# Performance work log

Measured on AMD Instinct MI355X. Metric: run time of the kernel, lower is better.

The kernel has to match this reference:

```python
import jax, jax.numpy as jnp
import numpy as np

D_MODEL, D_STATE, EXPAND = 256, 16, 2
D_INNER = EXPAND * D_MODEL
DT_RANK = (D_MODEL + 15) // 16
BATCH, SEQLEN = 4, 4096


def silu(x):
    return x * jax.nn.sigmoid(x)


def setup_inputs() -> dict:
    key = jax.random.key(0)
    ks = jax.random.split(key, 10)
    h = jax.random.normal(ks[0], (BATCH, SEQLEN, D_MODEL), dtype=jnp.float32)
    Wi_f = jax.random.normal(ks[1], (2 * D_INNER, D_MODEL), dtype=jnp.float32) / np.sqrt(D_MODEL)
    Wi_b = jax.random.normal(ks[2], (2 * D_INNER, D_MODEL), dtype=jnp.float32) / np.sqrt(D_MODEL)
    Wx_f = jax.random.normal(ks[3], (DT_RANK + 2 * D_STATE, D_INNER), dtype=jnp.float32) / np.sqrt(D_INNER)
    Wx_b = jax.random.normal(ks[4], (DT_RANK + 2 * D_STATE, D_INNER), dtype=jnp.float32) / np.sqrt(D_INNER)
    dt_std = DT_RANK ** -0.5
    Wdt_f = jax.random.uniform(ks[5], (D_INNER, DT_RANK), dtype=jnp.float32, minval=-dt_std, maxval=dt_std)
    Wdt_b = jax.random.uniform(ks[6], (D_INNER, DT_RANK), dtype=jnp.float32, minval=-dt_std, maxval=dt_std)
    # dt bias = inverse-softplus of dt sampled log-uniform in [1e-3, 1e-1]
    dt = jnp.exp(jax.random.uniform(ks[7], (D_INNER,), dtype=jnp.float32) * (np.log(0.1) - np.log(0.001)) + np.log(0.001))
    dt = jnp.clip(dt, 1e-4, None)
    inv_dt = dt + jnp.log(-jnp.expm1(-dt))
    bdt_f = inv_dt
    bdt_b = inv_dt
    A_log = jnp.log(jnp.broadcast_to(jnp.arange(1, D_STATE + 1, dtype=jnp.float32), (D_INNER, D_STATE)))
    A_log_f = A_log
    A_log_b = A_log
    D_f = jnp.ones((D_INNER,), dtype=jnp.float32)
    D_b = jnp.ones((D_INNER,), dtype=jnp.float32)
    Wo = jax.random.normal(ks[8], (D_MODEL, 2 * D_INNER), dtype=jnp.float32) / np.sqrt(2 * D_INNER)
    return {"hidden_states": h, "Wi_f": Wi_f, "Wi_b": Wi_b, "Wx_f": Wx_f, "Wx_b": Wx_b,
            "Wdt_f": Wdt_f, "Wdt_b": Wdt_b, "bdt_f": bdt_f, "bdt_b": bdt_b,
            "A_log_f": A_log_f, "A_log_b": A_log_b, "D_f": D_f, "D_b": D_b, "Wo": Wo}


def mamba_dir(h, Wi, Wx, Wdt, bdt, A_log, Dp, reverse):
    b, l, _ = h.shape
    di, r = Wdt.shape
    n = A_log.shape[1]
    xz = h @ Wi.T                      # [b,l,2*di]
    if reverse:
        xz = xz[:, ::-1]
    x, z = xz[..., :di], xz[..., di:]
    u = silu(x)                        # selective_scan input u
    x_dbl = u @ Wx.T                   # [b,l,r+2n]
    delta = jax.nn.softplus(x_dbl[..., :r] @ Wdt.T + bdt)   # [b,l,di]
    Bm = x_dbl[..., r:r + n]           # [b,l,n]
    Cm = x_dbl[..., r + n:r + 2 * n]   # [b,l,n]
    A = -jnp.exp(A_log)                # [di,n]

    def step(s, inp):
        u_t, d_t, B_t, C_t = inp       # [b,di],[b,di],[b,n],[b,n]
        dA = jnp.exp(d_t[..., None] * A)                         # [b,di,n]
        s = dA * s + (d_t * u_t)[..., None] * B_t[:, None, :]    # [b,di,n]
        y_t = jnp.einsum('bdn,bn->bd', s, C_t)
        return s, y_t

    s0 = jnp.zeros((b, di, n), dtype=u.dtype)
    xs = (jnp.swapaxes(u, 0, 1), jnp.swapaxes(delta, 0, 1),
          jnp.swapaxes(Bm, 0, 1), jnp.swapaxes(Cm, 0, 1))
    _, ys = jax.lax.scan(step, s0, xs)
    y = jnp.swapaxes(ys, 0, 1) + u * Dp          # skip term D*u
    y = y * silu(z)                              # gated output
    if reverse:
        y = y[:, ::-1]
    return y


def reference(hidden_states, Wi_f, Wi_b, Wx_f, Wx_b, Wdt_f, Wdt_b, bdt_f, bdt_b, A_log_f, A_log_b, D_f, D_b, Wo):
    y_f = mamba_dir(hidden_states, Wi_f, Wx_f, Wdt_f, bdt_f, A_log_f, D_f, False)
    y_b = mamba_dir(hidden_states, Wi_b, Wx_b, Wdt_b, bdt_b, A_log_b, D_b, True)
    y = jnp.concatenate([y_f, y_b], axis=-1)     # [b,l,2*di]
    return y @ Wo.T                              # [b,l,d_model]
```

## Files before the change

### kernel.cpp

```cpp
#include <hip/hip_runtime.h>
#include <hip/hip_bf16.h>
#include <cstddef>
#include <cstdint>

#define D_MODELc 256
#define D_STATEc 16
#define D_INNERc 512
#define DT_RANKc 16
#define BATCHc   4
#define SEQLENc  4096
#define NCHUNK   128
#define CHUNK    32

typedef unsigned short u16;
typedef __attribute__((ext_vector_type(8))) short bf16x8;
typedef __attribute__((ext_vector_type(4))) float f32x4;
typedef float __attribute__((ext_vector_type(4))) f4v;

__device__ __forceinline__ float siluf(float v) { return v / (1.f + __expf(-v)); }

__device__ __forceinline__ u16 bf16_rne(float f) {
    uint32_t u = __float_as_uint(f);
    u += 0x7fffu + ((u >> 16) & 1u);
    return (u16)(u >> 16);
}
__device__ __forceinline__ float bf16_to_f(u16 h) {
    return __uint_as_float(((uint32_t)h) << 16);
}
__device__ __forceinline__ uint32_t pack_hl(float f) {
    u16 hh = bf16_rne(f);
    u16 ll = bf16_rne(f - bf16_to_f(hh));
    return ((uint32_t)hh << 16) | ll;
}
__device__ __forceinline__ float unpack_add(uint32_t v) {
    return __uint_as_float(v & 0xFFFF0000u) + __uint_as_float(v << 16);
}
__device__ __forceinline__ void unpack_frag(const uint32_t* q, bf16x8& fh, bf16x8& fl) {
    union { bf16x8 v; uint32_t w[4]; } H, L;
    #pragma unroll
    for (int i = 0; i < 4; i++) {
        uint32_t a = q[2 * i], b = q[2 * i + 1];
        H.w[i] = (a >> 16) | (b & 0xFFFF0000u);
        L.w[i] = (a & 0xFFFFu) | (b << 16);
    }
    fh = H.v; fl = L.v;
}
__device__ __forceinline__ float softplusf(float x) {
    return fmaxf(x, 0.f) + __logf(1.f + __expf(-fabsf(x)));
}

#define GLL16(g, l) __builtin_amdgcn_global_load_lds( \
    (const __attribute__((address_space(1))) uint32_t*)(g), \
    (__attribute__((address_space(3))) uint32_t*)(l), 16, 0, 0)

__global__ __launch_bounds__(256) void split_kernel(const float* __restrict__ in,
                                                    u16* __restrict__ hi,
                                                    u16* __restrict__ lo, int n4) {
    int i = blockIdx.x * 256 + threadIdx.x;
    const int stride = gridDim.x * 256;
    for (; i < n4; i += stride) {
        float4 v = ((const float4*)in)[i];
        u16 h0 = bf16_rne(v.x), h1 = bf16_rne(v.y), h2 = bf16_rne(v.z), h3 = bf16_rne(v.w);
        ushort4 hv; hv.x = h0; hv.y = h1; hv.z = h2; hv.w = h3;
        ushort4 lv;
        lv.x = bf16_rne(v.x - bf16_to_f(h0));
        lv.y = bf16_rne(v.y - bf16_to_f(h1));
        lv.z = bf16_rne(v.z - bf16_to_f(h2));
        lv.w = bf16_rne(v.w - bf16_to_f(h3));
        ((ushort4*)hi)[i] = hv;
        ((ushort4*)lo)[i] = lv;
    }
}

template<int EPI, int NBL2, int AINT>
__global__ __launch_bounds__(256) void gemm_mfma(
        const u16* __restrict__ Ah, const u16* __restrict__ Al, int lda,
        const u16* __restrict__ Bh, const u16* __restrict__ Bl, int ldb,
        float* __restrict__ out0,
        uint32_t* __restrict__ uhl,
        int M, int N, int K) {
    __shared__ char lds[2][32768];
    const int t    = threadIdx.x;
    const int lane = t & 63;
    const int wid  = t >> 6;
    const int wrow = wid >> 1, wcol = wid & 1;

    const int id  = blockIdx.x;
    const int xcd = id & 7;
    const int j   = id >> 3;
    const int nb  = j & ((1 << NBL2) - 1);
    const int mg  = j >> NBL2;
    const int m0  = (mg * 8 + xcd) * 128;
    const int n0  = nb * 128;

    const int lr  = lane & 15;
    const int kgl = lane >> 4;

    f32x4 acc[4][4] = {};

    auto stage = [&](int buf, int k0) {
        if (AINT == 0) {
            #pragma unroll
            for (int i = 0; i < 8; i++) {
                int c    = i * 256 + t;
                int tile = c >> 9;
                int kg   = (c >> 7) & 3;
                int row  = c & 127;
                const u16* bsrc = (tile == 0) ? Ah : (tile == 1) ? Al : (tile == 2) ? Bh : Bl;
                int r0 = (tile < 2) ? m0 : n0;
                int ld = (tile < 2) ? lda : ldb;
                const u16* g = bsrc + (size_t)(r0 + row) * ld + k0 + kg * 8;
                GLL16(g, &lds[buf][c * 16]);
            }
        } else {
            const uint32_t* Aint = (const uint32_t*)Ah;
            #pragma unroll
            for (int i = 0; i < 8; i++) {
                int c = i * 256 + t;
                if (c < 1024) {
                    int kg   = c >> 8;
                    int row  = (c >> 1) & 127;
                    int half = c & 1;
                    const uint32_t* g = Aint + (size_t)(m0 + row) * lda + k0 + kg * 8 + half * 4;
                    GLL16(g, &lds[buf][c * 16]);
                } else {
                    int cb   = c - 1024;
                    int tile = cb >> 9;
                    int kg   = (cb >> 7) & 3;
                    int row  = cb & 127;
                    const u16* bsrc = tile ? Bl : Bh;
                    const u16* g = bsrc + (size_t)(n0 + row) * ldb + k0 + kg * 8;
                    GLL16(g, &lds[buf][c * 16]);
                }
            }
        }
    };

    const int NT = K >> 5;
    stage(0, 0);
    __syncthreads();

    for (int kt = 0; kt < NT; ++kt) {
        const int buf = kt & 1;
        if (kt + 1 < NT) stage(buf ^ 1, (kt + 1) * 32);

        bf16x8 afh[4], afl[4];
        if (AINT == 0) {
            const u16* lb = (const u16*)lds[buf];
            #pragma unroll
            for (int mi = 0; mi < 4; mi++) {
                int row = wrow * 64 + mi * 16 + lr;
                afh[mi] = *(const bf16x8*)(lb + 0 * 4096 + kgl * 1024 + row * 8);
                afl[mi] = *(const bf16x8*)(lb + 1 * 4096 + kgl * 1024 + row * 8);
            }
        } else {
            const uint32_t* la = (const uint32_t*)lds[buf];
            #pragma unroll
            for (int mi = 0; mi < 4; mi++) {
                int row = wrow * 64 + mi * 16 + lr;
                unpack_frag(la + kgl * 1024 + row * 8, afh[mi], afl[mi]);
            }
        }
        const u16* lbB = (const u16*)(lds[buf] + 16384);
        #pragma unroll
        for (int ni = 0; ni < 4; ni++) {
            int row = wcol * 64 + ni * 16 + lr;
            bf16x8 bfh = *(const bf16x8*)(lbB + 0 * 4096 + kgl * 1024 + row * 8);
            bf16x8 bfl = *(const bf16x8*)(lbB + 1 * 4096 + kgl * 1024 + row * 8);
            #pragma unroll
            for (int mi = 0; mi < 4; mi++) {
                acc[mi][ni] = __builtin_amdgcn_mfma_f32_16x16x32_bf16(afh[mi], bfh, acc[mi][ni], 0, 0, 0);
                acc[mi][ni] = __builtin_amdgcn_mfma_f32_16x16x32_bf16(afh[mi], bfl, acc[mi][ni], 0, 0, 0);
                acc[mi][ni] = __builtin_amdgcn_mfma_f32_16x16x32_bf16(afl[mi], bfh, acc[mi][ni], 0, 0, 0);
            }
        }
        __syncthreads();
    }

    #pragma unroll
    for (int mi = 0; mi < 4; mi++) {
        #pragma unroll
        for (int ni = 0; ni < 4; ni++) {
            #pragma unroll
            for (int r = 0; r < 4; r++) {
                int m = m0 + wrow * 64 + mi * 16 + kgl * 4 + r;
                int n = n0 + wcol * 64 + ni * 16 + lr;
                float v = acc[mi][ni][r];
                if (EPI == 0) {
                    __builtin_nontemporal_store(v, &out0[(size_t)m * N + n]);
                } else {
                    float s = siluf(v);
                    int dirn = n >> 10;
                    int nn   = n & 1023;
                    size_t dof = (size_t)dirn * (size_t)M * 512;
                    if (nn < 512) {
                        uhl[dof + (size_t)m * 512 + nn] = pack_hl(s);
                    } else {
                        out0[dof + (size_t)m * 512 + (nn - 512)] = s;
                    }
                }
            }
        }
    }
}

__global__ __launch_bounds__(256) void xdbl_mfma(
        const uint32_t* __restrict__ Uhl,
        const u16* __restrict__ WxH, const u16* __restrict__ WxL,
        float* __restrict__ out) {
    __shared__ uint32_t lds[4][64][8];
    const int t    = threadIdx.x;
    const int lane = t & 63;
    const int wid  = t >> 6;
    const int m0   = blockIdx.x * 64;
    const int dir  = blockIdx.y;
    const int Mp   = gridDim.x * 64;
    const int lr   = lane & 15;
    const int kgl  = lane >> 4;

    const size_t dofU = (size_t)dir * (size_t)Mp * 512;
    const size_t dofW = (size_t)dir * (size_t)48 * 512;

    f32x4 acc[3] = {};

    for (int k0 = 0; k0 < 512; k0 += 32) {
        #pragma unroll
        for (int i = 0; i < 2; i++) {
            int c    = i * 256 + t;
            int kg   = c >> 7;
            int row  = (c >> 1) & 63;
            int half = c & 1;
            const uint32_t* g = Uhl + dofU + (size_t)(m0 + row) * 512 + k0 + kg * 8 + half * 4;
            GLL16(g, ((char*)lds) + (size_t)c * 16);
        }
        __syncthreads();

        bf16x8 afh, afl;
        unpack_frag(&lds[kgl][wid * 16 + lr][0], afh, afl);
        #pragma unroll
        for (int nf = 0; nf < 3; nf++) {
            const size_t boff = dofW + (size_t)(nf * 16 + lr) * 512 + k0 + kgl * 8;
            bf16x8 bfh = *(const bf16x8*)(WxH + boff);
            bf16x8 bfl = *(const bf16x8*)(WxL + boff);
            acc[nf] = __builtin_amdgcn_mfma_f32_16x16x32_bf16(afh, bfh, acc[nf], 0, 0, 0);
            acc[nf] = __builtin_amdgcn_mfma_f32_16x16x32_bf16(afh, bfl, acc[nf], 0, 0, 0);
            acc[nf] = __builtin_amdgcn_mfma_f32_16x16x32_bf16(afl, bfh, acc[nf], 0, 0, 0);
        }
        __syncthreads();
    }

    float* o = out + (size_t)dir * (size_t)Mp * 48;
    #pragma unroll
    for (int nf = 0; nf < 3; nf++) {
        #pragma unroll
        for (int r = 0; r < 4; r++) {
            int m = m0 + wid * 16 + kgl * 4 + r;
            int n = nf * 16 + lr;
            o[(size_t)m * 48 + n] = acc[nf][r];
        }
    }
}

__global__ __launch_bounds__(256) void scan_phaseA(
        const uint32_t* __restrict__ Uhl,
        const float* __restrict__ XD,
        const float* __restrict__ Wdt_f, const float* __restrict__ Wdt_b,
        const float* __restrict__ bdt_f, const float* __restrict__ bdt_b,
        const float* __restrict__ AL_f, const float* __restrict__ AL_b,
        float* __restrict__ SDL, float* __restrict__ S) {
    const int c   = blockIdx.x;
    const int d   = blockIdx.y * 256 + threadIdx.x;
    const int z   = blockIdx.z;
    const int dir = z & 1;
    const int b   = z >> 1;
    const int PB  = gridDim.z >> 1;
    const int Mp  = PB * SEQLENc;
    const float* Wdt = dir ? Wdt_b : Wdt_f;
    const float* bdt = dir ? bdt_b : bdt_f;
    const float* AL  = dir ? AL_b  : AL_f;
    const uint32_t* UD = Uhl + (size_t)dir * Mp * 512;
    const float* XDD = XD + (size_t)dir * Mp * 48;

    float w[16], a[16], s[16];
    #pragma unroll
    for (int n = 0; n < 16; n++) {
        w[n] = Wdt[d * 16 + n];
        a[n] = -__expf(AL[d * 16 + n]);
        s[n] = 0.f;
    }
    const float a0 = a[0];
    bool pw = (a0 != 0.f);
    #pragma unroll
    for (int n = 1; n < 16; n++)
        pw = pw && (fabsf(a[n] - (float)(n + 1) * a0) <= 3e-6f * fabsf(a[n]));
    const float bb = bdt[d];
    float sdl = 0.f;

    for (int i = 0; i < CHUNK; i++) {
        int tt = c * CHUNK + i;
        int l  = dir ? (SEQLENc - 1 - tt) : tt;
        size_t row = (size_t)b * SEQLENc + l;
        float uu = unpack_add(UD[row * 512 + d]);
        const f4v* xr4 = (const f4v*)&XDD[row * 48];
        float acc = bb;
        #pragma unroll
        for (int k = 0; k < 4; k++) {
            f4v xa = xr4[k];
            acc += xa[0]*w[k*4+0] + xa[1]*w[k*4+1] + xa[2]*w[k*4+2] + xa[3]*w[k*4+3];
        }
        float dl = softplusf(acc);
        sdl += dl;
        float du = dl * uu;
        if (pw) {
            float q = __expf(a0 * dl);
            float dAn = 1.f;
            #pragma unroll
            for (int g = 0; g < 4; g++) {
                f4v B4 = xr4[4 + g];
                #pragma unroll
                for (int jj = 0; jj < 4; jj++) {
                    int n = g * 4 + jj;
                    dAn *= q;
                    s[n] = dAn * s[n] + du * B4[jj];
                }
            }
        } else {
            #pragma unroll
            for (int g = 0; g < 4; g++) {
                f4v B4 = xr4[4 + g];
                #pragma unroll
                for (int jj = 0; jj < 4; jj++) {
                    int n = g * 4 + jj;
                    float dA = __expf(dl * a[n]);
                    s[n] = dA * s[n] + du * B4[jj];
                }
            }
        }
    }
    SDL[((size_t)z * NCHUNK + c) * 512 + d] = sdl;
    size_t base = (((size_t)z * NCHUNK + c) * 16) * 512 + d;
    #pragma unroll
    for (int n = 0; n < 16; n++)
        S[base + (size_t)n * 512] = s[n];
}

__global__ __launch_bounds__(256) void scan_phaseB(const float* __restrict__ SDL,
                                                   float* __restrict__ S,
                                                   const float* __restrict__ AL_f,
                                                   const float* __restrict__ AL_b) {
    const int g   = blockIdx.x * 256 + threadIdx.x;
    const int d   = g & 511;
    const int n   = (g >> 9) & 15;
    const int z   = g >> 13;
    const int dir = z & 1;
    const float an = -__expf((dir ? AL_b : AL_f)[d * 16 + n]);
    const size_t strideS = (size_t)16 * 512;
    size_t offS = (((size_t)z * NCHUNK) * 16 + n) * 512 + d;
    size_t offD = ((size_t)z * NCHUNK) * 512 + d;
    float carry = 0.f;
    float sdl = SDL[offD], ss = S[offS];
    for (int c = 0; c < NCHUNK; c++) {
        float sdn = 0.f, sn = 0.f;
        if (c + 1 < NCHUNK) { sdn = SDL[offD + 512]; sn = S[offS + strideS]; }
        float pp = __expf(an * sdl);
        S[offS] = carry;
        carry = pp * carry + ss;
        sdl = sdn; ss = sn;
        offS += strideS; offD += 512;
    }
}

__global__ __launch_bounds__(256) void scan_phaseC(
        const uint32_t* __restrict__ Uhl,
        const float* __restrict__ XD,
        const float* __restrict__ Wdt_f, const float* __restrict__ Wdt_b,
        const float* __restrict__ bdt_f, const float* __restrict__ bdt_b,
        const float* __restrict__ AL_f, const float* __restrict__ AL_b,
        const float* __restrict__ E,
        const float* __restrict__ SZ,
        const float* __restrict__ D_f,  const float* __restrict__ D_b,
        uint32_t* __restrict__ Yhl) {
    const int c   = blockIdx.x;
    const int d   = blockIdx.y * 256 + threadIdx.x;
    const int z   = blockIdx.z;
    const int dir = z & 1;
    const int b   = z >> 1;
    const int PB  = gridDim.z >> 1;
    const int Mp  = PB * SEQLENc;
    const float* Wdt = dir ? Wdt_b : Wdt_f;
    const float* bdt = dir ? bdt_b : bdt_f;
    const float* AL  = dir ? AL_b  : AL_f;
    const uint32_t* UD = Uhl + (size_t)dir * Mp * 512;
    const float* XDD = XD + (size_t)dir * Mp * 48;
    const float* SZD = SZ + (size_t)dir * Mp * 512;

    float w[16], a[16], s[16];
    size_t base = (((size_t)z * NCHUNK + c) * 16) * 512 + d;
    #pragma unroll
    for (int n = 0; n < 16; n++) {
        w[n] = Wdt[d * 16 + n];
        a[n] = -__expf(AL[d * 16 + n]);
        s[n] = E[base + (size_t)n * 512];
    }
    const float a0 = a[0];
    bool pw = (a0 != 0.f);
    #pragma unroll
    for (int n = 1; n < 16; n++)
        pw = pw && (fabsf(a[n] - (float)(n + 1) * a0) <= 3e-6f * fabsf(a[n]));
    const float bb = bdt[d];
    const float Dd = (dir ? D_b : D_f)[d];

    for (int i = 0; i < CHUNK; i++) {
        int tt = c * CHUNK + i;
        int l  = dir ? (SEQLENc - 1 - tt) : tt;
        size_t row = (size_t)b * SEQLENc + l;
        float uu = unpack_add(UD[row * 512 + d]);
        const f4v* xr4 = (const f4v*)&XDD[row * 48];
        float acc = bb;
        #pragma unroll
        for (int k = 0; k < 4; k++) {
            f4v xa = xr4[k];
            acc += xa[0]*w[k*4+0] + xa[1]*w[k*4+1] + xa[2]*w[k*4+2] + xa[3]*w[k*4+3];
        }
        float dl = softplusf(acc);
        float du = dl * uu;
        float y = 0.f;
        if (pw) {
            float q = __expf(a0 * dl);
            float dAn = 1.f;
            #pragma unroll
            for (int g = 0; g < 4; g++) {
                f4v B4 = xr4[4 + g];
                f4v C4 = xr4[8 + g];
                #pragma unroll
                for (int jj = 0; jj < 4; jj++) {
                    int n = g * 4 + jj;
                    dAn *= q;
                    s[n] = dAn * s[n] + du * B4[jj];
                    y += s[n] * C4[jj];
                }
            }
        } else {
            #pragma unroll
            for (int g = 0; g < 4; g++) {
                f4v B4 = xr4[4 + g];
                f4v C4 = xr4[8 + g];
                #pragma unroll
                for (int jj = 0; jj < 4; jj++) {
                    int n = g * 4 + jj;
                    float dA = __expf(dl * a[n]);
                    s[n] = dA * s[n] + du * B4[jj];
                    y += s[n] * C4[jj];
                }
            }
        }
        float sz = SZD[row * 512 + d];
        float yv = (y + uu * Dd) * sz;
        Yhl[row * 1024 + (size_t)dir * 512 + d] = pack_hl(yv);
    }
}

extern "C" void kernel_launch(void* const* d_in, const int* in_sizes, int n_in,
                              void* d_out, int out_size, void* d_ws, size_t ws_size,
                              hipStream_t stream) {
    const float* h    = (const float*)d_in[0];
    const float* Wi_f = (const float*)d_in[1];
    const float* Wi_b = (const float*)d_in[2];
    const float* Wx_f = (const float*)d_in[3];
    const float* Wx_b = (const float*)d_in[4];
    const float* Wdt_f= (const float*)d_in[5];
    const float* Wdt_b= (const float*)d_in[6];
    const float* bdt_f= (const float*)d_in[7];
    const float* bdt_b= (const float*)d_in[8];
    const float* Al_f = (const float*)d_in[9];
    const float* Al_b = (const float*)d_in[10];
    const float* D_f  = (const float*)d_in[11];
    const float* D_b  = (const float*)d_in[12];
    const float* Wo   = (const float*)d_in[13];
    float* out = (float*)d_out;

    const size_t W_ELE  = 1024 * 256;
    const size_t WX_ELE = 48 * 512;
    const size_t FB   = (size_t)SEQLENc * D_INNERc;
    const size_t FH   = (size_t)SEQLENc * D_MODELc;
    const size_t FX   = (size_t)SEQLENc * 48;
    const size_t FP   = (size_t)NCHUNK * 16 * 512;
    const size_t FD   = (size_t)NCHUNK * 512;
    const size_t FY   = (size_t)SEQLENc * 1024;

    const size_t fixed_bytes = (8 * W_ELE + 4 * WX_ELE) * sizeof(u16);
    const size_t per_b = 2 * FH * sizeof(u16)
                       + 2 * FB * sizeof(float)
                       + 2 * FB * sizeof(uint32_t)
                       + 2 * FX * sizeof(float)
                       + 2 * (FP + FD) * sizeof(float)
                       + FY * sizeof(uint32_t);
    int PB = 4;
    if (fixed_bytes + 4 * per_b + 65536 > ws_size) PB = 2;
    if (fixed_bytes + 2 * per_b + 65536 > ws_size) PB = 1;

    char* cur = (char*)d_ws;
    auto alloc = [&](size_t bytes) -> char* {
        char* p = cur; cur += (bytes + 255) & ~(size_t)255; return p;
    };
    u16* WiH = (u16*)alloc(2 * W_ELE * 2);
    u16* WiL = (u16*)alloc(2 * W_ELE * 2);
    u16* WoH = (u16*)alloc(W_ELE * 2);
    u16* WoL = (u16*)alloc(W_ELE * 2);
    u16* WxH = (u16*)alloc(2 * WX_ELE * 2);
    u16* WxL = (u16*)alloc(2 * WX_ELE * 2);
    u16*      hH  = (u16*)alloc((size_t)PB * FH * 2);
    u16*      hL  = (u16*)alloc((size_t)PB * FH * 2);
    float*    sz  = (float*)alloc((size_t)PB * 2 * FB * 4);
    uint32_t* uhl = (uint32_t*)alloc((size_t)PB * 2 * FB * 4);
    float*    xd  = (float*)alloc((size_t)PB * 2 * FX * 4);
    float*    SDL = (float*)alloc((size_t)PB * 2 * FD * 4);
    float*    S   = (float*)alloc((size_t)PB * 2 * FP * 4);
    uint32_t* yhl = (uint32_t*)alloc((size_t)PB * FY * 4);

    {
        int n4 = (int)(W_ELE / 4);
        int blocks = (n4 + 255) / 256; if (blocks > 1024) blocks = 1024;
        split_kernel<<<blocks, 256, 0, stream>>>(Wi_f, WiH, WiL, n4);
        split_kernel<<<blocks, 256, 0, stream>>>(Wi_b, WiH + W_ELE, WiL + W_ELE, n4);
        split_kernel<<<blocks, 256, 0, stream>>>(Wo,   WoH, WoL, n4);
        int nx4 = (int)(WX_ELE / 4);
        split_kernel<<<(nx4 + 255) / 256, 256, 0, stream>>>(Wx_f, WxH, WxL, nx4);
        split_kernel<<<(nx4 + 255) / 256, 256, 0, stream>>>(Wx_b, WxH + WX_ELE, WxL + WX_ELE, nx4);
    }

    for (int b0 = 0; b0 < BATCHc; b0 += PB) {
        const int Mp = PB * SEQLENc;
        const int MB = Mp / 128;
        const float* hB = h   + (size_t)b0 * FH;
        float*       oB = out + (size_t)b0 * FH;

        {
            int n4 = (int)((size_t)PB * FH / 4);
            int blocks = (n4 + 255) / 256; if (blocks > 2048) blocks = 2048;
            split_kernel<<<blocks, 256, 0, stream>>>(hB, hH, hL, n4);
        }

        gemm_mfma<1, 4, 0><<<16 * MB, 256, 0, stream>>>(
            hH, hL, D_MODELc, WiH, WiL, D_MODELc,
            sz, uhl, Mp, 2048, D_MODELc);

        xdbl_mfma<<<dim3(Mp / 64, 2), 256, 0, stream>>>(uhl, WxH, WxL, xd);

        scan_phaseA<<<dim3(NCHUNK, 2, 2 * PB), 256, 0, stream>>>(
            uhl, xd, Wdt_f, Wdt_b, bdt_f, bdt_b, Al_f, Al_b, SDL, S);
        scan_phaseB<<<PB * 64, 256, 0, stream>>>(SDL, S, Al_f, Al_b);
        scan_phaseC<<<dim3(NCHUNK, 2, 2 * PB), 256, 0, stream>>>(
            uhl, xd, Wdt_f, Wdt_b, bdt_f, bdt_b, Al_f, Al_b,
            S, sz, D_f, D_b, yhl);

        gemm_mfma<0, 1, 1><<<2 * MB, 256, 0, stream>>>(
            (const u16*)yhl, nullptr, 1024, WoH, WoL, 1024,
            oB, nullptr, Mp, D_MODELc, 1024);
    }
}
```

Baseline: 349.9 us.

## Load GEMM A fragments directly from global and shorten scan dependency chains

The GEMM now stages only the B tiles in LDS, and each wave reads its A fragments straight from global memory into registers. This halves shared memory use and removes half the LDS traffic, at the cost of uncoalesced, unshared global reads of A. The scan kernels compute dt with a tree-reduced dot product and build the decay powers q^n with a logarithmic multiply ladder instead of a serial chain. The output dot product is split into four partial sums, which shortens the serial dependency chains per timestep.

Measured after the change: 389.7 us. 11.4% more time.

```diff
diff --git a/kernel.cpp b/kernel.cpp
--- a/kernel.cpp
+++ b/kernel.cpp
@@ -47,6 +47,26 @@
 }
 __device__ __forceinline__ float softplusf(float x) {
     return fmaxf(x, 0.f) + __logf(1.f + __expf(-fabsf(x)));
+}
+__device__ __forceinline__ float dot16_tree(const f4v x[4], const float* w, float bias) {
+    float t0 = fmaf(x[0][1], w[1],  x[0][0] * w[0]);
+    float t1 = fmaf(x[0][3], w[3],  x[0][2] * w[2]);
+    float t2 = fmaf(x[1][1], w[5],  x[1][0] * w[4]);
+    float t3 = fmaf(x[1][3], w[7],  x[1][2] * w[6]);
+    float t4 = fmaf(x[2][1], w[9],  x[2][0] * w[8]);
+    float t5 = fmaf(x[2][3], w[11], x[2][2] * w[10]);
+    float t6 = fmaf(x[3][1], w[13], x[3][2] * 0.f + x[3][0] * w[12]);
+    float t7 = fmaf(x[3][3], w[15], x[3][2] * w[14]);
+    return bias + (((t0 + t1) + (t2 + t3)) + ((t4 + t5) + (t6 + t7)));
+}
+__device__ __forceinline__ void qladder(float q, float* qd) {
+    float q2 = q * q;
+    float q4 = q2 * q2;
+    float q8 = q4 * q4;
+    qd[0] = q;        qd[1] = q2;       qd[2] = q2 * q;   qd[3] = q4;
+    qd[4] = q4 * q;   qd[5] = q4 * q2;  qd[6] = q4 * qd[2]; qd[7] = q8;
+    qd[8] = q8 * q;   qd[9] = q8 * q2;  qd[10] = q8 * qd[2]; qd[11] = q8 * q4;
+    qd[12] = q8 * qd[4]; qd[13] = q8 * qd[5]; qd[14] = q8 * qd[6]; qd[15] = q8 * q8;
 }
 
 #define GLL16(g, l) __builtin_amdgcn_global_load_lds( \
@@ -79,7 +99,7 @@
         float* __restrict__ out0,
         uint32_t* __restrict__ uhl,
         int M, int N, int K) {
-    __shared__ char lds[2][32768];
+    __shared__ u16 ldsB[2][2][4][128][8];
     const int t    = threadIdx.x;
     const int lane = t & 63;
     const int wid  = t >> 6;
@@ -98,75 +118,46 @@
 
     f32x4 acc[4][4] = {};
 
-    auto stage = [&](int buf, int k0) {
-        if (AINT == 0) {
-            #pragma unroll
-            for (int i = 0; i < 8; i++) {
-                int c    = i * 256 + t;
-                int tile = c >> 9;
-                int kg   = (c >> 7) & 3;
-                int row  = c & 127;
-                const u16* bsrc = (tile == 0) ? Ah : (tile == 1) ? Al : (tile == 2) ? Bh : Bl;
-                int r0 = (tile < 2) ? m0 : n0;
-                int ld = (tile < 2) ? lda : ldb;
-                const u16* g = bsrc + (size_t)(r0 + row) * ld + k0 + kg * 8;
-                GLL16(g, &lds[buf][c * 16]);
-            }
-        } else {
-            const uint32_t* Aint = (const uint32_t*)Ah;
-            #pragma unroll
-            for (int i = 0; i < 8; i++) {
-                int c = i * 256 + t;
-                if (c < 1024) {
-                    int kg   = c >> 8;
-                    int row  = (c >> 1) & 127;
-                    int half = c & 1;
-                    const uint32_t* g = Aint + (size_t)(m0 + row) * lda + k0 + kg * 8 + half * 4;
-                    GLL16(g, &lds[buf][c * 16]);
-                } else {
-                    int cb   = c - 1024;
-                    int tile = cb >> 9;
-                    int kg   = (cb >> 7) & 3;
-                    int row  = cb & 127;
-                    const u16* bsrc = tile ? Bl : Bh;
-                    const u16* g = bsrc + (size_t)(n0 + row) * ldb + k0 + kg * 8;
-                    GLL16(g, &lds[buf][c * 16]);
-                }
-            }
+    auto stageB = [&](int buf, int k0) {
+        #pragma unroll
+        for (int i = 0; i < 4; i++) {
+            int c    = i * 256 + t;
+            int tile = c >> 9;
+            int kg   = (c >> 7) & 3;
+            int row  = c & 127;
+            const u16* bsrc = tile ? Bl : Bh;
+            const u16* g = bsrc + (size_t)(n0 + row) * ldb + k0 + kg * 8;
+            GLL16(g, ((char*)ldsB) + (size_t)buf * 16384 + (size_t)c * 16);
         }
     };
 
     const int NT = K >> 5;
-    stage(0, 0);
+    stageB(0, 0);
     __syncthreads();
 
     for (int kt = 0; kt < NT; ++kt) {
         const int buf = kt & 1;
-        if (kt + 1 < NT) stage(buf ^ 1, (kt + 1) * 32);
+        if (kt + 1 < NT) stageB(buf ^ 1, (kt + 1) * 32);
 
         bf16x8 afh[4], afl[4];
-        if (AINT == 0) {
-            const u16* lb = (const u16*)lds[buf];
-            #pragma unroll
-            for (int mi = 0; mi < 4; mi++) {
-                int row = wrow * 64 + mi * 16 + lr;
-                afh[mi] = *(const bf16x8*)(lb + 0 * 4096 + kgl * 1024 + row * 8);
-                afl[mi] = *(const bf16x8*)(lb + 1 * 4096 + kgl * 1024 + row * 8);
-            }
-        } else {
-            const uint32_t* la = (const uint32_t*)lds[buf];
-            #pragma unroll
-            for (int mi = 0; mi < 4; mi++) {
-                int row = wrow * 64 + mi * 16 + lr;
-                unpack_frag(la + kgl * 1024 + row * 8, afh[mi], afl[mi]);
-            }
-        }
-        const u16* lbB = (const u16*)(lds[buf] + 16384);
+        const int k0 = kt * 32;
+        #pragma unroll
+        for (int mi = 0; mi < 4; mi++) {
+            int row = m0 + wrow * 64 + mi * 16 + lr;
+            if (AINT == 0) {
+                afh[mi] = *(const bf16x8*)(Ah + (size_t)row * lda + k0 + kgl * 8);
+                afl[mi] = *(const bf16x8*)(Al + (size_t)row * lda + k0 + kgl * 8);
+            } else {
+                const uint32_t* Aint = (const uint32_t*)Ah;
+                unpack_frag(Aint + (size_t)row * lda + k0 + kgl * 8, afh[mi], afl[mi]);
+            }
+        }
+
         #pragma unroll
         for (int ni = 0; ni < 4; ni++) {
             int row = wcol * 64 + ni * 16 + lr;
-            bf16x8 bfh = *(const bf16x8*)(lbB + 0 * 4096 + kgl * 1024 + row * 8);
-            bf16x8 bfl = *(const bf16x8*)(lbB + 1 * 4096 + kgl * 1024 + row * 8);
+            bf16x8 bfh = *(const bf16x8*)&ldsB[buf][0][kgl][row][0];
+            bf16x8 bfl = *(const bf16x8*)&ldsB[buf][1][kgl][row][0];
             #pragma unroll
             for (int mi = 0; mi < 4; mi++) {
                 acc[mi][ni] = __builtin_amdgcn_mfma_f32_16x16x32_bf16(afh[mi], bfh, acc[mi][ni], 0, 0, 0);
@@ -302,26 +293,20 @@
         size_t row = (size_t)b * SEQLENc + l;
         float uu = unpack_add(UD[row * 512 + d]);
         const f4v* xr4 = (const f4v*)&XDD[row * 48];
-        float acc = bb;
-        #pragma unroll
-        for (int k = 0; k < 4; k++) {
-            f4v xa = xr4[k];
-            acc += xa[0]*w[k*4+0] + xa[1]*w[k*4+1] + xa[2]*w[k*4+2] + xa[3]*w[k*4+3];
-        }
-        float dl = softplusf(acc);
+        f4v xw[4] = {xr4[0], xr4[1], xr4[2], xr4[3]};
+        float dl = softplusf(dot16_tree(xw, w, bb));
         sdl += dl;
         float du = dl * uu;
         if (pw) {
-            float q = __expf(a0 * dl);
-            float dAn = 1.f;
+            float qd[16];
+            qladder(__expf(a0 * dl), qd);
             #pragma unroll
             for (int g = 0; g < 4; g++) {
                 f4v B4 = xr4[4 + g];
                 #pragma unroll
                 for (int jj = 0; jj < 4; jj++) {
                     int n = g * 4 + jj;
-                    dAn *= q;
-                    s[n] = dAn * s[n] + du * B4[jj];
+                    s[n] = fmaf(qd[n], s[n], du * B4[jj]);
                 }
             }
         } else {
@@ -332,7 +317,7 @@
                 for (int jj = 0; jj < 4; jj++) {
                     int n = g * 4 + jj;
                     float dA = __expf(dl * a[n]);
-                    s[n] = dA * s[n] + du * B4[jj];
+                    s[n] = fmaf(dA, s[n], du * B4[jj]);
                 }
             }
         }
@@ -416,44 +401,45 @@
         size_t row = (size_t)b * SEQLENc + l;
         float uu = unpack_add(UD[row * 512 + d]);
         const f4v* xr4 = (const f4v*)&XDD[row * 48];
-        float acc = bb;
-        #pragma unroll
-        for (int k = 0; k < 4; k++) {
-            f4v xa = xr4[k];
-            acc += xa[0]*w[k*4+0] + xa[1]*w[k*4+1] + xa[2]*w[k*4+2] + xa[3]*w[k*4+3];
-        }
-        float dl = softplusf(acc);
+        f4v xw[4] = {xr4[0], xr4[1], xr4[2], xr4[3]};
+        float dl = softplusf(dot16_tree(xw, w, bb));
         float du = dl * uu;
-        float y = 0.f;
+        float yp0 = 0.f, yp1 = 0.f, yp2 = 0.f, yp3 = 0.f;
         if (pw) {
-            float q = __expf(a0 * dl);
-            float dAn = 1.f;
+            float qd[16];
+            qladder(__expf(a0 * dl), qd);
             #pragma unroll
             for (int g = 0; g < 4; g++) {
                 f4v B4 = xr4[4 + g];
                 f4v C4 = xr4[8 + g];
+                float yp = 0.f;
                 #pragma unroll
                 for (int jj = 0; jj < 4; jj++) {
                     int n = g * 4 + jj;
-                    dAn *= q;
-                    s[n] = dAn * s[n] + du * B4[jj];
-                    y += s[n] * C4[jj];
+                    s[n] = fmaf(qd[n], s[n], du * B4[jj]);
+                    yp = fmaf(s[n], C4[jj], yp);
                 }
+                if (g == 0) yp0 = yp; else if (g == 1) yp1 = yp;
+                else if (g == 2) yp2 = yp; else yp3 = yp;
             }
         } else {
             #pragma unroll
             for (int g = 0; g < 4; g++) {
                 f4v B4 = xr4[4 + g];
                 f4v C4 = xr4[8 + g];
+                float yp = 0.f;
                 #pragma unroll
                 for (int jj = 0; jj < 4; jj++) {
                     int n = g * 4 + jj;
                     float dA = __expf(dl * a[n]);
-                    s[n] = dA * s[n] + du * B4[jj];
-                    y += s[n] * C4[jj];
+                    s[n] = fmaf(dA, s[n], du * B4[jj]);
+                    yp = fmaf(s[n], C4[jj], yp);
                 }
-            }
-        }
+                if (g == 0) yp0 = yp; else if (g == 1) yp1 = yp;
+                else if (g == 2) yp2 = yp; else yp3 = yp;
+            }
+        }
+        float y = (yp0 + yp1) + (yp2 + yp3);
         float sz = SZD[row * 512 + d];
         float yv = (y + uu * Dd) * sz;
         Yhl[row * 1024 + (size_t)dir * 512 + d] = pack_hl(yv);
```
